# Performance work log

Measured on AMD Instinct MI355X. Metric: run time of the kernel, lower is better.

Reference implementation:

```python
import jax, jax.numpy as jnp
import numpy as np

D_MODEL = 512
N_HEADS = 16
D_HEAD = D_MODEL // N_HEADS
SQRT_DIM = float(np.sqrt(D_MODEL))


def _rel_shift(pos_score):
    # Transformer-XL relative shift: pad a zero column, reshape, drop first row.
    b, h, s1, s2 = pos_score.shape
    padded = jnp.pad(pos_score, ((0, 0), (0, 0), (0, 0), (1, 0)))  # [b,h,s1,s2+1]
    padded = padded.reshape(b, h, s2 + 1, s1)
    return padded[:, :, 1:].reshape(b, h, s1, s2)


def setup_inputs() -> dict:
    key = jax.random.key(0)
    ks = jax.random.split(key, 16)
    B, S = 2, 2048
    inp = {
        "query": jax.random.normal(ks[0], (B, S, D_MODEL), jnp.float32),
        "key": jax.random.normal(ks[1], (B, S, D_MODEL), jnp.float32),
        "value": jax.random.normal(ks[2], (B, S, D_MODEL), jnp.float32),
        "pos_embedding": jax.random.normal(ks[3], (B, S, D_MODEL), jnp.float32),
        "mask": jnp.zeros((B, 1, S), jnp.bool_),
    }
    sc = 1.0 / np.sqrt(D_MODEL)
    inp["Wq"] = jax.random.normal(ks[4], (D_MODEL, D_MODEL), jnp.float32) * sc
    inp["bq"] = jnp.zeros((D_MODEL,), jnp.float32)
    inp["Wk"] = jax.random.normal(ks[5], (D_MODEL, D_MODEL), jnp.float32) * sc
    inp["bk"] = jnp.zeros((D_MODEL,), jnp.float32)
    inp["Wv"] = jax.random.normal(ks[6], (D_MODEL, D_MODEL), jnp.float32) * sc
    inp["bv"] = jnp.zeros((D_MODEL,), jnp.float32)
    inp["Wpos"] = jax.random.normal(ks[7], (D_MODEL, D_MODEL), jnp.float32) * sc
    inp["u_bias"] = jax.random.normal(ks[8], (N_HEADS, D_HEAD), jnp.float32) * sc
    inp["v_bias"] = jax.random.normal(ks[9], (N_HEADS, D_HEAD), jnp.float32) * sc
    inp["Wo"] = jax.random.normal(ks[10], (D_MODEL, D_MODEL), jnp.float32) * sc
    inp["bo"] = jnp.zeros((D_MODEL,), jnp.float32)
    return inp


def reference(query, key, value, pos_embedding, mask,
              Wq, bq, Wk, bk, Wv, bv, Wpos, u_bias, v_bias, Wo, bo):
    B = value.shape[0]
    # projections (torch Linear: x @ W.T + b); reshape to [b, s, h, d]
    q = (jnp.einsum('bsd,ed->bse', query, Wq) + bq).reshape(B, -1, N_HEADS, D_HEAD)
    k = (jnp.einsum('bsd,ed->bse', key, Wk) + bk).reshape(B, -1, N_HEADS, D_HEAD)
    v = (jnp.einsum('bsd,ed->bse', value, Wv) + bv).reshape(B, -1, N_HEADS, D_HEAD)
    pe = jnp.einsum('bsd,ed->bse', pos_embedding, Wpos).reshape(B, -1, N_HEADS, D_HEAD)
    # content score: (q + u) @ k^T  -> [b, h, s, s]
    content_score = jnp.einsum('bqhd,bkhd->bhqk', q + u_bias, k)
    # pos score: (q + v_bias) @ pe^T, then relative shift
    pos_score = _rel_shift(jnp.einsum('bqhd,bkhd->bhqk', q + v_bias, pe))
    score = (content_score + pos_score) / SQRT_DIM
    score = jnp.where(mask[:, None], -1e9, score)  # mask: [b,1,s] -> [b,1,1,s]
    attn = jax.nn.softmax(score, axis=-1)
    # dropout with p=0.0 in eval mode: identity
    context = jnp.einsum('bhqk,bkhd->bqhd', attn, v).reshape(B, -1, D_MODEL)
    out = jnp.einsum('bsd,ed->bse', context, Wo) + bo
    return (out, attn)
```

## Files before the change

### kernel.cpp

```cpp
#include <hip/hip_runtime.h>
#include <hip/hip_bf16.h>

#define B_ 2
#define H_ 16
#define S_ 2048
#define D_ 32
#define DM_ 512
#define SCW 2052

typedef __attribute__((ext_vector_type(8))) short short8;
typedef __attribute__((ext_vector_type(4))) float f32x4;

__device__ __forceinline__ unsigned short f2bf(float f) {
    unsigned int u = __builtin_bit_cast(unsigned int, f);
    unsigned int r = (u + 0x7fffu + ((u >> 16) & 1u)) >> 16;
    return (unsigned short)r;
}
__device__ __forceinline__ float bf2f(unsigned short s) {
    unsigned int u = ((unsigned int)s) << 16;
    return __builtin_bit_cast(float, u);
}

__device__ __forceinline__ void gemm64_tile(const float* __restrict__ X,
                                            const float* __restrict__ W,
                                            int row0, int col0,
                                            unsigned short* ldsA,
                                            unsigned short* ldsB,
                                            f32x4 acc[2][2]) {
    const int tid = threadIdx.x;
    const int w = tid >> 6, l = tid & 63, lr = l & 15, lg = l >> 4;
    const int wr = w >> 1, wc = w & 1;
    const int sr = tid >> 2, seg = tid & 3;

    for (int kt = 0; kt < 16; ++kt) {
        int k0 = kt * 32;
        __syncthreads();
        {
            const float* ap = X + (size_t)(row0 + sr) * DM_ + k0 + seg * 8;
            float4 a0 = *(const float4*)ap;
            float4 a1 = *(const float4*)(ap + 4);
            short8 av;
            av[0] = (short)f2bf(a0.x); av[1] = (short)f2bf(a0.y);
            av[2] = (short)f2bf(a0.z); av[3] = (short)f2bf(a0.w);
            av[4] = (short)f2bf(a1.x); av[5] = (short)f2bf(a1.y);
            av[6] = (short)f2bf(a1.z); av[7] = (short)f2bf(a1.w);
            *(short8*)(ldsA + sr * 40 + seg * 8) = av;

            const float* bp = W + (size_t)(col0 + sr) * DM_ + k0 + seg * 8;
            float4 b0 = *(const float4*)bp;
            float4 b1 = *(const float4*)(bp + 4);
            short8 bv;
            bv[0] = (short)f2bf(b0.x); bv[1] = (short)f2bf(b0.y);
            bv[2] = (short)f2bf(b0.z); bv[3] = (short)f2bf(b0.w);
            bv[4] = (short)f2bf(b1.x); bv[5] = (short)f2bf(b1.y);
            bv[6] = (short)f2bf(b1.z); bv[7] = (short)f2bf(b1.w);
            *(short8*)(ldsB + sr * 40 + seg * 8) = bv;
        }
        __syncthreads();
        short8 af0 = *(short8*)(ldsA + (32 * wr + lr) * 40 + lg * 8);
        short8 af1 = *(short8*)(ldsA + (32 * wr + 16 + lr) * 40 + lg * 8);
        short8 bf0 = *(short8*)(ldsB + (32 * wc + lr) * 40 + lg * 8);
        short8 bf1 = *(short8*)(ldsB + (32 * wc + 16 + lr) * 40 + lg * 8);
        acc[0][0] = __builtin_amdgcn_mfma_f32_16x16x32_bf16(af0, bf0, acc[0][0], 0, 0, 0);
        acc[0][1] = __builtin_amdgcn_mfma_f32_16x16x32_bf16(af0, bf1, acc[0][1], 0, 0, 0);
        acc[1][0] = __builtin_amdgcn_mfma_f32_16x16x32_bf16(af1, bf0, acc[1][0], 0, 0, 0);
        acc[1][1] = __builtin_amdgcn_mfma_f32_16x16x32_bf16(af1, bf1, acc[1][1], 0, 0, 0);
    }
}

__global__ __launch_bounds__(256) void proj_kernel(
    const float* __restrict__ q_in, const float* __restrict__ k_in,
    const float* __restrict__ v_in, const float* __restrict__ p_in,
    const float* __restrict__ Wq, const float* __restrict__ Wk,
    const float* __restrict__ Wv, const float* __restrict__ Wp,
    const float* __restrict__ bq, const float* __restrict__ bk,
    const float* __restrict__ bv,
    const float* __restrict__ ub, const float* __restrict__ vb,
    unsigned short* __restrict__ quB, unsigned short* __restrict__ qvB,
    unsigned short* __restrict__ kB, unsigned short* __restrict__ peB,
    unsigned short* __restrict__ vtB) {
    __shared__ unsigned short ldsA[64 * 40];
    __shared__ unsigned short ldsB[64 * 40];

    const int mode = blockIdx.z;
    const float* X = (mode == 0) ? q_in : (mode == 1) ? k_in : (mode == 2) ? v_in : p_in;
    const float* W = (mode == 0) ? Wq : (mode == 1) ? Wk : (mode == 2) ? Wv : Wp;
    const float* bias = (mode == 0) ? bq : (mode == 1) ? bk : (mode == 2) ? bv : nullptr;

    const int row0 = blockIdx.x * 64, col0 = blockIdx.y * 64;
    f32x4 acc[2][2];
    for (int i = 0; i < 2; ++i)
        for (int j = 0; j < 2; ++j)
            acc[i][j] = (f32x4){0.f, 0.f, 0.f, 0.f};

    gemm64_tile(X, W, row0, col0, ldsA, ldsB, acc);

    const int tid = threadIdx.x;
    const int w = tid >> 6, l = tid & 63, lr = l & 15, lg = l >> 4;
    const int wr = w >> 1, wc = w & 1;

    for (int i = 0; i < 2; ++i) {
        for (int j = 0; j < 2; ++j) {
            int colg = col0 + 32 * wc + 16 * j + lr;
            int h = colg >> 5, d = colg & 31;
            float bb = bias ? bias[colg] : 0.f;
            int rbase = row0 + 32 * wr + 16 * i + 4 * lg;
            if (mode == 2) {
                int b = rbase >> 11;
                int s0 = rbase & 2047;
                ushort4 pk;
                pk.x = f2bf(acc[i][j][0] + bb);
                pk.y = f2bf(acc[i][j][1] + bb);
                pk.z = f2bf(acc[i][j][2] + bb);
                pk.w = f2bf(acc[i][j][3] + bb);
                size_t o = ((size_t)((b * H_ + h) * D_ + d)) * S_ + s0;
                *(ushort4*)(vtB + o) = pk;
            } else {
                float ubv = 0.f, vbv = 0.f;
                if (mode == 0) { ubv = ub[colg]; vbv = vb[colg]; }
                for (int e = 0; e < 4; ++e) {
                    int rg = rbase + e;
                    int b = rg >> 11, s = rg & 2047;
                    size_t o = ((size_t)((b * H_ + h) * S_ + s)) * D_ + d;
                    float y = acc[i][j][e] + bb;
                    if (mode == 0) {
                        quB[o] = f2bf(y + ubv);
                        qvB[o] = f2bf(y + vbv);
                    } else if (mode == 1) {
                        kB[o] = f2bf(y);
                    } else {
                        peB[o] = f2bf(y);
                    }
                }
            }
        }
    }
}

__global__ __launch_bounds__(512, 4) void attn_kernel(
    const unsigned short* __restrict__ quB, const unsigned short* __restrict__ qvB,
    const unsigned short* __restrict__ kB, const unsigned short* __restrict__ peB,
    const unsigned short* __restrict__ vtB, const unsigned char* __restrict__ mask,
    float* __restrict__ attn_out, float* __restrict__ ctx) {
    __shared__ unsigned short sc[16 * SCW];
    __shared__ float wsum[8 * 16];
    __shared__ float rowli[16];

    const int tid = threadIdx.x, w = tid >> 6, lr = tid & 15, lg = (tid & 63) >> 4;
    const int id = blockIdx.x + 128 * blockIdx.y + 2048 * blockIdx.z;
    const int swz = (id & 7) * 512 + (id >> 3);
    const int q0 = (swz & 127) * 16;
    const int h = (swz >> 7) & 15;
    const int b = swz >> 11;
    const size_t headoff = ((size_t)(b * H_ + h)) * S_ * D_;
    const float SCALE = 0.044194173824159216f;
    const unsigned short* peH = peB + headoff;

    short8 qu_f = *(const short8*)(quB + headoff + (size_t)(q0 + lr) * D_ + lg * 8);
    short8 qvA_f = *(const short8*)(qvB + headoff + (size_t)(q0 + lr) * D_ + lg * 8);
    int rBq = q0 + 1 + lr; if (rBq > S_ - 1) rBq = S_ - 1;
    short8 qvB_f = *(const short8*)(qvB + headoff + (size_t)rBq * D_ + lg * 8);

    if (tid < 16) sc[tid * SCW + q0 + tid + 1] = 0;

    {
        const int ntA = q0 / 16 + 1;
        auto ldA = [&](int ju) -> short8 {
            int t = (ju < ntA) ? ju : (ntA - 1);
            int pr = S_ - 16 - q0 + 16 * t + lr;
            if (pr > S_ - 1) pr = S_ - 1;
            return *(const short8*)(peH + (size_t)pr * D_ + lg * 8);
        };
        auto scatA = [&](int ju, short8 pf) {
            f32x4 dd = (f32x4){0.f, 0.f, 0.f, 0.f};
            dd = __builtin_amdgcn_mfma_f32_16x16x32_bf16(pf, qvA_f, dd, 0, 0, 0);
            int u0 = 16 * ju;
            #pragma unroll
            for (int i = 0; i < 4; ++i) {
                int u = u0 + 4 * lg + i;
                if (u >= 15 - lr) sc[lr * SCW + (lr + u - 15)] = f2bf(dd[i] * SCALE);
            }
        };
        short8 f0 = ldA(w), f1 = ldA(w + 8);
        for (int ju = w; ju < ntA; ju += 16) {
            short8 f2 = ldA(ju + 16);
            short8 f3 = ldA(ju + 24);
            scatA(ju, f0);
            if (ju + 8 < ntA) scatA(ju + 8, f1);
            f0 = f2; f1 = f3;
        }
    }
    {
        const int ntB = (S_ - q0) / 16;
        auto ldB = [&](int ju) -> short8 {
            int t = (ju < ntB) ? ju : (ntB - 1);
            int pr = 16 * t + lr - 2;
            if (pr < 0) pr = 0;
            return *(const short8*)(peH + (size_t)pr * D_ + lg * 8);
        };
        auto scatB = [&](int ju, short8 pf) {
            f32x4 dd = (f32x4){0.f, 0.f, 0.f, 0.f};
            dd = __builtin_amdgcn_mfma_f32_16x16x32_bf16(pf, qvB_f, dd, 0, 0, 0);
            int u0 = 16 * ju;
            #pragma unroll
            for (int i = 0; i < 4; ++i) {
                int u = u0 + 4 * lg + i;
                int c = q0 + lr + u;
                if (u >= 2 && c <= S_ - 1) sc[lr * SCW + c] = f2bf(dd[i] * SCALE);
            }
        };
        short8 f0 = ldB(w), f1 = ldB(w + 8);
        for (int ju = w; ju < ntB; ju += 16) {
            short8 f2 = ldB(ju + 16);
            short8 f3 = ldB(ju + 24);
            scatB(ju, f0);
            if (ju + 8 < ntB) scatB(ju + 8, f1);
            f0 = f2; f1 = f3;
        }
    }
    __syncthreads();

    float rs = 0.f;
    {
        const unsigned char* mrow = mask + b * S_;
        const unsigned short* kH = kB + headoff;
        #pragma unroll
        for (int t = 0; t < 16; ++t) {
            const int j = w + 8 * t;
            short8 kf = *(const short8*)(kH + (size_t)(16 * j + lr) * D_ + lg * 8);
            unsigned int mk4 = *(const unsigned int*)(mrow + 16 * j + 4 * lg);
            f32x4 dd = (f32x4){0.f, 0.f, 0.f, 0.f};
            dd = __builtin_amdgcn_mfma_f32_16x16x32_bf16(kf, qu_f, dd, 0, 0, 0);
            unsigned short* p = sc + lr * SCW + 16 * j + 4 * lg;
            ushort4 pv = *(ushort4*)p;
            float e0 = __expf(bf2f(pv.x) + dd[0] * SCALE + ((mk4 & 0xffu) ? -1e9f : 0.f));
            float e1 = __expf(bf2f(pv.y) + dd[1] * SCALE + ((mk4 & 0xff00u) ? -1e9f : 0.f));
            float e2 = __expf(bf2f(pv.z) + dd[2] * SCALE + ((mk4 & 0xff0000u) ? -1e9f : 0.f));
            float e3 = __expf(bf2f(pv.w) + dd[3] * SCALE + ((mk4 & 0xff000000u) ? -1e9f : 0.f));
            rs += (e0 + e1) + (e2 + e3);
            ushort4 ov;
            ov.x = f2bf(e0); ov.y = f2bf(e1); ov.z = f2bf(e2); ov.w = f2bf(e3);
            *(ushort4*)p = ov;
        }
    }
    rs += __shfl_xor(rs, 16);
    rs += __shfl_xor(rs, 32);
    if ((tid & 63) < 16) wsum[w * 16 + lr] = rs;
    __syncthreads();
    if (tid < 16) {
        float t = 0.f;
        #pragma unroll
        for (int ww = 0; ww < 8; ++ww) t += wsum[ww * 16 + tid];
        rowli[tid] = 1.0f / t;
    }
    __syncthreads();

    if (w < 2) {
        f32x4 acc = (f32x4){0.f, 0.f, 0.f, 0.f};
        const unsigned short* vb2 = vtB + ((size_t)(b * H_ + h)) * D_ * S_ +
                                    (size_t)(16 * w + lr) * S_;
        #pragma unroll 8
        for (int ks = 0; ks < 64; ++ks) {
            int koff = 32 * ks;
            short8 af = *(short8*)(sc + lr * SCW + koff + lg * 8);
            short8 bf = *(const short8*)(vb2 + koff + lg * 8);
            acc = __builtin_amdgcn_mfma_f32_16x16x32_bf16(af, bf, acc, 0, 0, 0);
        }
        #pragma unroll
        for (int i = 0; i < 4; ++i) {
            int q = 4 * lg + i;
            ctx[((size_t)(b * S_ + q0 + q)) * DM_ + h * D_ + 16 * w + lr] =
                acc[i] * rowli[q];
        }
    } else {
        int tt = tid - 128;
        float* abase = attn_out + ((size_t)((b * H_ + h) * S_ + q0)) * S_;
        for (int idx = tt; idx < 16 * 512; idx += 384) {
            int r2 = idx >> 9, c4 = idx & 511;
            float li = rowli[r2];
            ushort4 s4 = *(ushort4*)(sc + r2 * SCW + c4 * 4);
            f32x4 av;
            av[0] = bf2f(s4.x) * li;
            av[1] = bf2f(s4.y) * li;
            av[2] = bf2f(s4.z) * li;
            av[3] = bf2f(s4.w) * li;
            __builtin_nontemporal_store(av, (f32x4*)(abase + (size_t)r2 * S_ + c4 * 4));
        }
    }
}

__global__ __launch_bounds__(256) void outproj_kernel(
    const float* __restrict__ ctx, const float* __restrict__ Wo,
    const float* __restrict__ bo, float* __restrict__ outp) {
    __shared__ unsigned short ldsA[64 * 40];
    __shared__ unsigned short ldsB[64 * 40];
    const int row0 = blockIdx.x * 64, col0 = blockIdx.y * 64;
    f32x4 acc[2][2];
    for (int i = 0; i < 2; ++i)
        for (int j = 0; j < 2; ++j)
            acc[i][j] = (f32x4){0.f, 0.f, 0.f, 0.f};
    gemm64_tile(ctx, Wo, row0, col0, ldsA, ldsB, acc);
    const int tid = threadIdx.x;
    const int w = tid >> 6, l = tid & 63, lr = l & 15, lg = l >> 4;
    const int wr = w >> 1, wc = w & 1;
    for (int i = 0; i < 2; ++i) {
        for (int j = 0; j < 2; ++j) {
            int colg = col0 + 32 * wc + 16 * j + lr;
            float bb = bo[colg];
            int rbase = row0 + 32 * wr + 16 * i + 4 * lg;
            for (int e = 0; e < 4; ++e) {
                outp[(size_t)(rbase + e) * DM_ + colg] = acc[i][j][e] + bb;
            }
        }
    }
}

extern "C" void kernel_launch(void* const* d_in, const int* in_sizes, int n_in,
                              void* d_out, int out_size, void* d_ws, size_t ws_size,
                              hipStream_t stream) {
    const float* q_in = (const float*)d_in[0];
    const float* k_in = (const float*)d_in[1];
    const float* v_in = (const float*)d_in[2];
    const float* p_in = (const float*)d_in[3];
    const unsigned char* mask = (const unsigned char*)d_in[4];
    const float* Wq = (const float*)d_in[5];
    const float* bq = (const float*)d_in[6];
    const float* Wk = (const float*)d_in[7];
    const float* bk = (const float*)d_in[8];
    const float* Wv = (const float*)d_in[9];
    const float* bv = (const float*)d_in[10];
    const float* Wp = (const float*)d_in[11];
    const float* ub = (const float*)d_in[12];
    const float* vb = (const float*)d_in[13];
    const float* Wo = (const float*)d_in[14];
    const float* bo = (const float*)d_in[15];

    char* ws = (char*)d_ws;
    const size_t BUF = 1u << 22;
    unsigned short* quB = (unsigned short*)(ws);
    unsigned short* qvB = (unsigned short*)(ws + BUF);
    unsigned short* kB  = (unsigned short*)(ws + 2 * BUF);
    unsigned short* peB = (unsigned short*)(ws + 3 * BUF);
    unsigned short* vtB = (unsigned short*)(ws + 4 * BUF);
    float* ctx = (float*)(ws + 5 * BUF);

    float* outp = (float*)d_out;
    float* attn = outp + (size_t)B_ * S_ * DM_;

    hipLaunchKernelGGL(proj_kernel, dim3(64, 8, 4), dim3(256), 0, stream,
                       q_in, k_in, v_in, p_in, Wq, Wk, Wv, Wp, bq, bk, bv,
                       ub, vb, quB, qvB, kB, peB, vtB);
    hipLaunchKernelGGL(attn_kernel, dim3(S_ / 16, H_, B_), dim3(512), 0, stream,
                       quB, qvB, kB, peB, vtB, mask, attn, ctx);
    hipLaunchKernelGGL(outproj_kernel, dim3(64, 8, 1), dim3(256), 0, stream,
                       ctx, Wo, bo, outp);
}
```

Baseline: 210.3 us.

## Use packed bf16 converts, exp2 with folded log2e, unmasked interior scatters

```diff
diff --git a/kernel.cpp b/kernel.cpp
--- a/kernel.cpp
+++ b/kernel.cpp
@@ -19,6 +19,17 @@
 __device__ __forceinline__ float bf2f(unsigned short s) {
     unsigned int u = ((unsigned int)s) << 16;
     return __builtin_bit_cast(float, u);
+}
+__device__ __forceinline__ unsigned int pkbf(float a, float b) {
+    unsigned int r;
+    asm("v_cvt_pk_bf16_f32 %0, %1, %2" : "=v"(r) : "v"(a), "v"(b));
+    return r;
+}
+__device__ __forceinline__ float bf2f_lo(unsigned int u) {
+    return __builtin_bit_cast(float, u << 16);
+}
+__device__ __forceinline__ float bf2f_hi(unsigned int u) {
+    return __builtin_bit_cast(float, u & 0xffff0000u);
 }
 
 __device__ __forceinline__ void gemm64_tile(const float* __restrict__ X,
@@ -153,7 +164,7 @@
     const int h = (swz >> 7) & 15;
     const int b = swz >> 11;
     const size_t headoff = ((size_t)(b * H_ + h)) * S_ * D_;
-    const float SCALE = 0.044194173824159216f;
+    const float SC2 = 0.044194173824159216f * 1.4426950408889634f;
     const unsigned short* peH = peB + headoff;
 
     short8 qu_f = *(const short8*)(quB + headoff + (size_t)(q0 + lr) * D_ + lg * 8);
@@ -174,11 +185,20 @@
         auto scatA = [&](int ju, short8 pf) {
             f32x4 dd = (f32x4){0.f, 0.f, 0.f, 0.f};
             dd = __builtin_amdgcn_mfma_f32_16x16x32_bf16(pf, qvA_f, dd, 0, 0, 0);
-            int u0 = 16 * ju;
-            #pragma unroll
-            for (int i = 0; i < 4; ++i) {
-                int u = u0 + 4 * lg + i;
-                if (u >= 15 - lr) sc[lr * SCW + (lr + u - 15)] = f2bf(dd[i] * SCALE);
+            unsigned int p01 = pkbf(dd[0] * SC2, dd[1] * SC2);
+            unsigned int p23 = pkbf(dd[2] * SC2, dd[3] * SC2);
+            int u0 = 16 * ju + 4 * lg;
+            int base = lr * SCW + lr + u0 - 15;
+            if (ju != 0) {
+                sc[base] = (unsigned short)p01;
+                sc[base + 1] = (unsigned short)(p01 >> 16);
+                sc[base + 2] = (unsigned short)p23;
+                sc[base + 3] = (unsigned short)(p23 >> 16);
+            } else {
+                if (u0 >= 15 - lr)     sc[base]     = (unsigned short)p01;
+                if (u0 + 1 >= 15 - lr) sc[base + 1] = (unsigned short)(p01 >> 16);
+                if (u0 + 2 >= 15 - lr) sc[base + 2] = (unsigned short)p23;
+                if (u0 + 3 >= 15 - lr) sc[base + 3] = (unsigned short)(p23 >> 16);
             }
         };
         short8 f0 = ldA(w), f1 = ldA(w + 8);
@@ -201,12 +221,21 @@
         auto scatB = [&](int ju, short8 pf) {
             f32x4 dd = (f32x4){0.f, 0.f, 0.f, 0.f};
             dd = __builtin_amdgcn_mfma_f32_16x16x32_bf16(pf, qvB_f, dd, 0, 0, 0);
-            int u0 = 16 * ju;
-            #pragma unroll
-            for (int i = 0; i < 4; ++i) {
-                int u = u0 + 4 * lg + i;
-                int c = q0 + lr + u;
-                if (u >= 2 && c <= S_ - 1) sc[lr * SCW + c] = f2bf(dd[i] * SCALE);
+            unsigned int p01 = pkbf(dd[0] * SC2, dd[1] * SC2);
+            unsigned int p23 = pkbf(dd[2] * SC2, dd[3] * SC2);
+            int u0 = 16 * ju + 4 * lg;
+            int c0 = q0 + lr + u0;
+            int base = lr * SCW + c0;
+            if (ju != 0 && ju != ntB - 1) {
+                sc[base] = (unsigned short)p01;
+                sc[base + 1] = (unsigned short)(p01 >> 16);
+                sc[base + 2] = (unsigned short)p23;
+                sc[base + 3] = (unsigned short)(p23 >> 16);
+            } else {
+                if (u0 >= 2 && c0 <= S_ - 1)         sc[base]     = (unsigned short)p01;
+                if (u0 + 1 >= 2 && c0 + 1 <= S_ - 1) sc[base + 1] = (unsigned short)(p01 >> 16);
+                if (u0 + 2 >= 2 && c0 + 2 <= S_ - 1) sc[base + 2] = (unsigned short)p23;
+                if (u0 + 3 >= 2 && c0 + 3 <= S_ - 1) sc[base + 3] = (unsigned short)(p23 >> 16);
             }
         };
         short8 f0 = ldB(w), f1 = ldB(w + 8);
@@ -231,16 +260,21 @@
             unsigned int mk4 = *(const unsigned int*)(mrow + 16 * j + 4 * lg);
             f32x4 dd = (f32x4){0.f, 0.f, 0.f, 0.f};
             dd = __builtin_amdgcn_mfma_f32_16x16x32_bf16(kf, qu_f, dd, 0, 0, 0);
-            unsigned short* p = sc + lr * SCW + 16 * j + 4 * lg;
-            ushort4 pv = *(ushort4*)p;
-            float e0 = __expf(bf2f(pv.x) + dd[0] * SCALE + ((mk4 & 0xffu) ? -1e9f : 0.f));
-            float e1 = __expf(bf2f(pv.y) + dd[1] * SCALE + ((mk4 & 0xff00u) ? -1e9f : 0.f));
-            float e2 = __expf(bf2f(pv.z) + dd[2] * SCALE + ((mk4 & 0xff0000u) ? -1e9f : 0.f));
-            float e3 = __expf(bf2f(pv.w) + dd[3] * SCALE + ((mk4 & 0xff000000u) ? -1e9f : 0.f));
+            unsigned int* p = (unsigned int*)(sc + lr * SCW + 16 * j + 4 * lg);
+            uint2 pq = *(uint2*)p;
+            float a0 = bf2f_lo(pq.x) + dd[0] * SC2 + ((mk4 & 0xffu) ? -1e9f : 0.f);
+            float a1 = bf2f_hi(pq.x) + dd[1] * SC2 + ((mk4 & 0xff00u) ? -1e9f : 0.f);
+            float a2 = bf2f_lo(pq.y) + dd[2] * SC2 + ((mk4 & 0xff0000u) ? -1e9f : 0.f);
+            float a3 = bf2f_hi(pq.y) + dd[3] * SC2 + ((mk4 & 0xff000000u) ? -1e9f : 0.f);
+            float e0 = __builtin_amdgcn_exp2f(a0);
+            float e1 = __builtin_amdgcn_exp2f(a1);
+            float e2 = __builtin_amdgcn_exp2f(a2);
+            float e3 = __builtin_amdgcn_exp2f(a3);
             rs += (e0 + e1) + (e2 + e3);
-            ushort4 ov;
-            ov.x = f2bf(e0); ov.y = f2bf(e1); ov.z = f2bf(e2); ov.w = f2bf(e3);
-            *(ushort4*)p = ov;
+            uint2 ov;
+            ov.x = pkbf(e0, e1);
+            ov.y = pkbf(e2, e3);
+            *(uint2*)p = ov;
         }
     }
     rs += __shfl_xor(rs, 16);
@@ -275,6 +309,7 @@
     } else {
         int tt = tid - 128;
         float* abase = attn_out + ((size_t)((b * H_ + h) * S_ + q0)) * S_;
+        #pragma unroll 8
         for (int idx = tt; idx < 16 * 512; idx += 384) {
             int r2 = idx >> 9, c4 = idx & 511;
             float li = rowli[r2];
@@ -284,7 +319,7 @@
             av[1] = bf2f(s4.y) * li;
             av[2] = bf2f(s4.z) * li;
             av[3] = bf2f(s4.w) * li;
-            __builtin_nontemporal_store(av, (f32x4*)(abase + (size_t)r2 * S_ + c4 * 4));
+            *(f32x4*)(abase + (size_t)r2 * S_ + c4 * 4) = av;
         }
     }
 }
```

New measurement: 250.3 us. 1.19x slower.
